# Kernel optimization log

Hardware: AMD Instinct MI355X
Metric: run time of the kernel (lower is better)

Reference implementation:

```python
import jax, jax.numpy as jnp
from jax import lax
import numpy as np

DEPTH = 4
D_MODEL = 192
D_INNER = 384
D_STATE = 16
D_CONV = 4
DT_RANK = 12
STRIDE = 4
NUM_PATCHES = 400
L_SEQ = NUM_PATCHES + 1  # +1 cls token appended at the end
EPS = 1e-5


def _rmsnorm(x, w):
    x = x.astype(jnp.float32)
    return (x * lax.rsqrt(jnp.mean(x * x, axis=-1, keepdims=True) + EPS)) * w


def _mamba(x, in_w, cw, cb, xp_w, dtw, dtb, A_log, Dv, ow):
    # x: [B, L, D_MODEL]
    B = x.shape[0]
    xz = jnp.einsum('bld,ed->ble', x, in_w)            # [B, L, 2*D_INNER]
    u, z = jnp.split(xz, 2, axis=-1)                   # [B, L, D_INNER] each
    # causal depthwise conv over L
    u_t = jnp.transpose(u, (0, 2, 1))                  # [B, D_INNER, L]
    u_pad = jnp.pad(u_t, ((0, 0), (0, 0), (D_CONV - 1, 0)))
    conv = lax.conv_general_dilated(
        u_pad, cw[:, None, :], (1,), 'VALID',
        dimension_numbers=('NCH', 'OIH', 'NCH'),
        feature_group_count=D_INNER)                   # [B, D_INNER, L]
    u = jax.nn.silu(conv + cb[:, None])
    u = jnp.transpose(u, (0, 2, 1))                    # [B, L, D_INNER]
    xdbl = jnp.einsum('bld,ed->ble', u, xp_w)          # [B, L, 44]
    dt, Bm, Cm = jnp.split(xdbl, [DT_RANK, DT_RANK + D_STATE], axis=-1)
    dt = jax.nn.softplus(jnp.einsum('blr,dr->bld', dt, dtw) + dtb)  # [B, L, D_INNER]
    A = -jnp.exp(A_log)                                # [D_INNER, D_STATE]
    dA = jnp.exp(dt[..., None] * A)                    # [B, L, D_INNER, D_STATE]
    dBu = dt[..., None] * Bm[:, :, None, :] * u[..., None]
    h0 = jnp.zeros((B, D_INNER, D_STATE), dtype=dA.dtype)

    def step(h, inp):
        dA_t, dBu_t = inp
        h = dA_t * h + dBu_t
        return h, h

    _, hs = lax.scan(step, h0, (jnp.swapaxes(dA, 0, 1), jnp.swapaxes(dBu, 0, 1)))
    hs = jnp.swapaxes(hs, 0, 1)                        # [B, L, D_INNER, D_STATE]
    y = jnp.einsum('bldn,bln->bld', hs, Cm) + u * Dv
    y = y * jax.nn.silu(z)
    return jnp.einsum('bld,ed->ble', y, ow)            # [B, L, D_MODEL]


def _forward(imgs, patch_w, patch_b, pos_embed, cls_token, norm_w, in_proj_w,
             conv_w, conv_b, xproj_w, dt_w, dt_b, A_log, D_param, out_w,
             normf_w, head_w, head_b):
    B = imgs.shape[0]
    # StrideEmbed: non-overlapping strides of 4 bytes -> linear to embed_dim
    x = imgs.reshape(B, NUM_PATCHES, STRIDE) @ patch_w + patch_b  # [B, 400, 192]
    x = x + pos_embed[:, :-1, :]
    cls = cls_token + pos_embed[:, -1:, :]             # [1, 1, 192]
    x = jnp.concatenate([x, jnp.broadcast_to(cls, (B, 1, D_MODEL))], axis=1)
    hidden = x
    residual = None
    for i in range(DEPTH):
        residual = hidden if residual is None else hidden + residual  # fp32 residual stream
        h = _rmsnorm(residual, norm_w[i])
        hidden = _mamba(h, in_proj_w[i], conv_w[i], conv_b[i], xproj_w[i],
                        dt_w[i], dt_b[i], A_log[i], D_param[i], out_w[i])
    x = _rmsnorm(hidden + residual, normf_w)
    cls_out = x[:, -1, :]                              # [B, 192]
    logits = cls_out @ head_w.T + head_b               # [B, 1000]
    return logits


def setup_inputs() -> dict:
    key = jax.random.key(0)
    ks = jax.random.split(key, 16)
    B = 32
    rn = lambda k, s, sc: jax.random.normal(k, s, dtype=jnp.float32) * sc
    A_log = jnp.broadcast_to(jnp.log(jnp.arange(1.0, D_STATE + 1.0, dtype=jnp.float32)),
                             (DEPTH, D_INNER, D_STATE))
    return {
        'imgs': rn(ks[0], (B, 1, 40, 40), 1.0),
        'patch_w': rn(ks[1], (STRIDE, D_MODEL), 0.1),
        'patch_b': jnp.zeros((D_MODEL,), jnp.float32),
        'pos_embed': rn(ks[2], (1, L_SEQ, D_MODEL), 0.02),
        'cls_token': rn(ks[3], (1, 1, D_MODEL), 0.02),
        'norm_w': jnp.ones((DEPTH, D_MODEL), jnp.float32),
        'in_proj_w': rn(ks[4], (DEPTH, 2 * D_INNER, D_MODEL), 0.05),
        'conv_w': rn(ks[5], (DEPTH, D_INNER, D_CONV), 0.3),
        'conv_b': jnp.zeros((DEPTH, D_INNER), jnp.float32),
        'xproj_w': rn(ks[6], (DEPTH, DT_RANK + 2 * D_STATE, D_INNER), 0.05),
        'dt_w': rn(ks[7], (DEPTH, D_INNER, DT_RANK), 0.1),
        'dt_b': rn(ks[8], (DEPTH, D_INNER), 0.5) - 4.0,
        'A_log': A_log,
        'D_param': jnp.ones((DEPTH, D_INNER), jnp.float32),
        'out_w': rn(ks[9], (DEPTH, D_MODEL, D_INNER), 0.05),
        'normf_w': jnp.ones((D_MODEL,), jnp.float32),
        'head_w': rn(ks[10], (1000, D_MODEL), 0.05),
        'head_b': jnp.zeros((1000,), jnp.float32),
    }


def reference(imgs, patch_w, patch_b, pos_embed, cls_token, norm_w, in_proj_w,
              conv_w, conv_b, xproj_w, dt_w, dt_b, A_log, D_param, out_w,
              normf_w, head_w, head_b):
    return _forward(imgs, patch_w, patch_b, pos_embed, cls_token, norm_w,
                    in_proj_w, conv_w, conv_b, xproj_w, dt_w, dt_b, A_log,
                    D_param, out_w, normf_w, head_w, head_b)
```

## Files before the change

### kernel.cpp

```cpp
#include <hip/hip_runtime.h>
#include <hip/hip_bf16.h>

#define B_SZ 32
#define LSEQ 401
#define NT (B_SZ * LSEQ)
#define DM 192
#define DI 384
#define DS 16
#define EPSF 1e-5f
#define ST 40
#define STP 44
#define NCH 8
#define PQN 1376256

typedef __attribute__((ext_vector_type(8))) short short8;
typedef __attribute__((ext_vector_type(4))) float f32x4;
typedef __hip_bfloat16 bf16;

#define OFF_IMGS    0
#define OFF_PATCHW  51200
#define OFF_PATCHB  51968
#define OFF_POS     52160
#define OFF_CLS     129152
#define OFF_NORMW   129344
#define OFF_INW     130112
#define OFF_CONVW   719936
#define OFF_CONVB   726080
#define OFF_XPROJW  727616
#define OFF_DTW     795200
#define OFF_DTB     813632
#define OFF_ALOG    815168
#define OFF_DP      839744
#define OFF_OUTW    841280
#define OFF_NORMF   1136192
#define OFF_HEADW   1136384
#define OFF_HEADB   1328384
#define OFF_TOTAL   1329384

#define WB_INW   0
#define WB_XPJ   589824
#define WB_OUT   688128
#define WB_DTW   983040
#define WB_TOTAL 1032192

__device__ __forceinline__ int chunk_s(int c) { return c == 0 ? 0 : c * 50 + 1; }
__device__ __forceinline__ int chunk_e(int c) { return (c + 1) * 50 + 1; }

__device__ __forceinline__ float ldsrc(const void* p, int off, int isbf) {
  return isbf ? __bfloat162float(((const bf16*)p)[off]) : ((const float*)p)[off];
}
__device__ __forceinline__ float fast_silu(float z) {
  return z * __builtin_amdgcn_rcpf(1.f + __expf(-z));
}
__device__ __forceinline__ float fast_softplus(float x) {
  float e = __expf(x);
  return (x > 15.f) ? x : __logf(1.f + e);
}

#define DPP_ADD(x, ctrl) \
  x += __int_as_float(__builtin_amdgcn_update_dpp(0, __float_as_int(x), ctrl, 0xF, 0xF, true))
__device__ __forceinline__ float row_sum16(float x) {
  DPP_ADD(x, 0xB1);
  DPP_ADD(x, 0x4E);
  DPP_ADD(x, 0x124);
  DPP_ADD(x, 0x128);
  return x;
}

struct P18 { const void* p[18]; };

__global__ __launch_bounds__(256) void k_convwb(P18 t, float* __restrict__ fin,
                                                bf16* __restrict__ wb) {
  static const int st[19] = {OFF_IMGS, OFF_PATCHW, OFF_PATCHB, OFF_POS, OFF_CLS,
                             OFF_NORMW, OFF_INW, OFF_CONVW, OFF_CONVB, OFF_XPROJW,
                             OFF_DTW, OFF_DTB, OFF_ALOG, OFF_DP, OFF_OUTW,
                             OFF_NORMF, OFF_HEADW, OFF_HEADB, OFF_TOTAL};
  int isbf = (((const unsigned short*)t.p[5])[0] == 0x3F80) ? 1 : 0;
  int idx = blockIdx.x * 256 + threadIdx.x;
  if (idx < OFF_TOTAL) {
    int lo = 0;
#pragma unroll
    for (int i = 1; i < 18; ++i) if (idx >= st[i]) lo = i;
    fin[idx] = ldsrc(t.p[lo], idx - st[lo], isbf);
  } else if (idx < OFF_TOTAL + WB_TOTAL) {
    int j = idx - OFF_TOTAL;
    float v;
    if (j < WB_XPJ) {
      v = ldsrc(t.p[6], j, isbf);
    } else if (j < WB_OUT) {
      int i2 = j - WB_XPJ;
      int l = i2 / (64 * 384);
      int r = (i2 / 384) & 63;
      int k = i2 % 384;
      v = (r < 44) ? ldsrc(t.p[9], l * 44 * 384 + r * 384 + k, isbf) : 0.f;
    } else if (j < WB_DTW) {
      v = ldsrc(t.p[14], j - WB_OUT, isbf);
    } else {
      int i2 = j - WB_DTW;
      int l = i2 / (384 * 32);
      int r = i2 % (384 * 32);
      int d = r >> 5;
      int k = r & 31;
      v = (k < 12) ? ldsrc(t.p[10], l * 4608 + d * 12 + k, isbf) : 0.f;
    }
    wb[j] = __float2bfloat16(v);
  }
}

__device__ __forceinline__ void inproj32(const bf16 (*shb)[200],
                                         const bf16* __restrict__ Win,
                                         bf16* __restrict__ xb,
                                         bf16* __restrict__ zb,
                                         int row0, int tid) {
  int lane = tid & 63, wave = tid >> 6;
  int q = lane >> 4, mlo = lane & 15;
  short8 afrA[6], afrB[6];
#pragma unroll
  for (int kk = 0; kk < 6; ++kk) {
    afrA[kk] = *(const short8*)&shb[mlo][kk * 32 + q * 8];
    afrB[kk] = *(const short8*)&shb[16 + mlo][kk * 32 + q * 8];
  }
  const bf16* wbase = Win + (size_t)(wave * 96 + mlo) * DM + q * 8;
#pragma unroll
  for (int jh = 0; jh < 2; ++jh) {
    short8 Bb[18];
#pragma unroll
    for (int j = 0; j < 3; ++j)
#pragma unroll
      for (int kk = 0; kk < 6; ++kk)
        Bb[j * 6 + kk] = *(const short8*)(wbase + (size_t)(jh * 3 + j) * 16 * DM + kk * 32);
#pragma unroll
    for (int j = 0; j < 3; ++j) {
      f32x4 aA = {}, aB = {};
#pragma unroll
      for (int kk = 0; kk < 6; ++kk) {
        aA = __builtin_amdgcn_mfma_f32_16x16x32_bf16(afrA[kk], Bb[j * 6 + kk], aA, 0, 0, 0);
        aB = __builtin_amdgcn_mfma_f32_16x16x32_bf16(afrB[kk], Bb[j * 6 + kk], aB, 0, 0, 0);
      }
      int n = wave * 96 + (jh * 3 + j) * 16 + mlo;
      if (n < DI) {
#pragma unroll
        for (int i = 0; i < 4; ++i) {
          xb[(size_t)(row0 + q * 4 + i) * DI + n] = __float2bfloat16(aA[i]);
          xb[(size_t)(row0 + 16 + q * 4 + i) * DI + n] = __float2bfloat16(aB[i]);
        }
      } else {
        int nz = n - DI;
#pragma unroll
        for (int i = 0; i < 4; ++i) {
          zb[(size_t)(row0 + q * 4 + i) * DI + nz] = __float2bfloat16(aA[i]);
          zb[(size_t)(row0 + 16 + q * 4 + i) * DI + nz] = __float2bfloat16(aB[i]);
        }
      }
    }
  }
}

__global__ __launch_bounds__(512, 2) void k_embedin(const float* __restrict__ fin,
                                                    float* __restrict__ residual,
                                                    const bf16* __restrict__ Win,
                                                    bf16* __restrict__ xb,
                                                    bf16* __restrict__ zb) {
  __shared__ bf16 shb[32][200];
  const float* imgs = fin + OFF_IMGS;
  const float* pw   = fin + OFF_PATCHW;
  const float* pb   = fin + OFF_PATCHB;
  const float* pos  = fin + OFF_POS;
  const float* cls  = fin + OFF_CLS;
  const float* nw0  = fin + OFF_NORMW;
  int tid = threadIdx.x;
  int row0 = blockIdx.x * 32;
  {
    int row = tid >> 4, g = tid & 15;
    int t = row0 + row;
    int b = t / LSEQ, l = t % LSEQ;
    float im[4];
    if (l < 400) {
#pragma unroll
      for (int s = 0; s < 4; ++s) im[s] = imgs[b * 1600 + l * 4 + s];
    }
    float rn[12], ss = 0.f;
#pragma unroll
    for (int k = 0; k < 12; ++k) {
      int col = g + 16 * k;
      float v;
      if (l < 400) {
        v = pb[col] + pos[l * DM + col];
#pragma unroll
        for (int s = 0; s < 4; ++s) v = fmaf(im[s], pw[s * DM + col], v);
      } else {
        v = cls[col] + pos[400 * DM + col];
      }
      residual[(size_t)t * DM + col] = v;
      rn[k] = v;
      ss = fmaf(v, v, ss);
    }
    ss = row_sum16(ss);
    float sres = rsqrtf(ss / (float)DM + EPSF);
#pragma unroll
    for (int k = 0; k < 12; ++k) {
      int col = g + 16 * k;
      shb[row][col] = __float2bfloat16(rn[k] * sres * nw0[col]);
    }
  }
  __syncthreads();
  inproj32(shb, Win, xb, zb, row0, tid);
}

__global__ __launch_bounds__(512) void k_xdt(const bf16* __restrict__ xb,
                                             const float* __restrict__ cw,
                                             const float* __restrict__ cb,
                                             const bf16* __restrict__ Wbf,
                                             float* __restrict__ xdbl,
                                             const bf16* __restrict__ dtwb,
                                             const float* __restrict__ dtb,
                                             bf16* __restrict__ ub,
                                             bf16* __restrict__ dto) {
  __shared__ bf16  sxt[19][392];
  __shared__ bf16  su[16][392];
  __shared__ float4 scw4[384];
  __shared__ float scb[384];
  __shared__ float sxp[2][16][48];
  __shared__ bf16  sxb[16][32];
  int row0 = blockIdx.x * 16;
  int tid = threadIdx.x;
  for (int i = tid; i < 19 * 48; i += 512) {
    int r = i / 48, c8 = i - r * 48;
    int t = row0 - 3 + r;
    if (t < 0) t = 0;
    *(short8*)&sxt[r][c8 * 8] = *(const short8*)(xb + (size_t)t * DI + c8 * 8);
  }
  for (int i = tid; i < 384; i += 512) {
    scw4[i] = ((const float4*)cw)[i];
    scb[i] = cb[i];
  }
  __syncthreads();
  for (int i = tid; i < 768; i += 512) {
    int tok = i / 48;
    int c8 = i - tok * 48;
    int d0 = c8 * 8;
    int t = row0 + tok;
    int l = t % LSEQ;
    float xr[4][8];
#pragma unroll
    for (int k = 0; k < 4; ++k) {
      short8 v = *(const short8*)&sxt[tok + k][d0];
      bool ok = (l - 3 + k) >= 0;
#pragma unroll
      for (int j = 0; j < 8; ++j) {
        unsigned int uu = ((unsigned int)(unsigned short)v[j]) << 16;
        xr[k][j] = ok ? __uint_as_float(uu) : 0.f;
      }
    }
    short8 uvv;
#pragma unroll
    for (int j = 0; j < 8; ++j) {
      float4 w = scw4[d0 + j];
      float a = scb[d0 + j];
      a = fmaf(xr[0][j], w.x, a);
      a = fmaf(xr[1][j], w.y, a);
      a = fmaf(xr[2][j], w.z, a);
      a = fmaf(xr[3][j], w.w, a);
      bf16 h = __float2bfloat16(fast_silu(a));
      uvv[j] = *reinterpret_cast<short*>(&h);
    }
    *(short8*)&su[tok][d0] = uvv;
    *(short8*)(ub + (size_t)t * DI + d0) = uvv;
  }
  __syncthreads();
  int lane = tid & 63;
  int wave = tid >> 6;
  int q = lane >> 4;
  int mlo = lane & 15;
  if (wave < 6) {
    int colw = (wave % 3) * 16;
    int kh = wave / 3;
    f32x4 acc = {};
    for (int k0 = 0; k0 < 192; k0 += 32) {
      short8 a = *(const short8*)&su[mlo][kh * 192 + k0 + q * 8];
      short8 b = *(const short8*)(Wbf + (size_t)(colw + mlo) * DI + kh * 192 + k0 + q * 8);
      acc = __builtin_amdgcn_mfma_f32_16x16x32_bf16(a, b, acc, 0, 0, 0);
    }
#pragma unroll
    for (int i = 0; i < 4; ++i) sxp[kh][q * 4 + i][colw + mlo] = acc[i];
  }
  __syncthreads();
  for (int i = tid; i < 16 * 44; i += 512) {
    int r = i / 44, c = i - r * 44;
    xdbl[(size_t)(row0 + r) * 44 + c] = sxp[0][r][c] + sxp[1][r][c];
  }
  for (int i = tid; i < 512; i += 512) {
    int tok = i >> 5, k = i & 31;
    sxb[tok][k] = __float2bfloat16(k < 12 ? sxp[0][tok][k] + sxp[1][tok][k] : 0.f);
  }
  __syncthreads();
  short8 afrag = *(const short8*)&sxb[mlo][q * 8];
#pragma unroll
  for (int jt = 0; jt < 3; ++jt) {
    int d = (wave * 3 + jt) * 16 + mlo;
    short8 bfrag = *(const short8*)(dtwb + (size_t)d * 32 + q * 8);
    f32x4 acc = {};
    acc = __builtin_amdgcn_mfma_f32_16x16x32_bf16(afrag, bfrag, acc, 0, 0, 0);
    float dtbv = dtb[d];
#pragma unroll
    for (int i = 0; i < 4; ++i)
      dto[(size_t)(row0 + q * 4 + i) * DI + d] =
          __float2bfloat16(fast_softplus(acc[i] + dtbv));
  }
}

__global__ __launch_bounds__(512) void k_scanA(const bf16* __restrict__ ub,
                                               const bf16* __restrict__ dtv,
                                               const float* __restrict__ xdbl,
                                               const float* __restrict__ A_log,
                                               float* __restrict__ Pq) {
  __shared__ float sdt[32][STP], sw[32][STP], sB[16][STP];
  int bx = blockIdx.x, b = blockIdx.y, c = blockIdx.z;
  int d0 = bx * 32;
  int tid = threadIdx.x;
  int dloc = tid >> 4, n = tid & 15;
  float A = -__expf(A_log[(d0 + dloc) * DS + n]);
  float S = 0.f, h = 0.f;
  int base = b * LSEQ;
  int lt = tid >> 5, lj = tid & 31;
  int s = chunk_s(c), e = chunk_e(c);
  for (int t0 = s; t0 < e; t0 += ST) {
    int tc = min(ST, e - t0);
    for (int tt = lt; tt < tc; tt += 16) {
      int g = base + t0 + tt;
      float dv = __bfloat162float(dtv[(size_t)g * DI + d0 + lj]);
      sdt[lj][tt] = dv;
      sw[lj][tt] = dv * __bfloat162float(ub[(size_t)g * DI + d0 + lj]);
      if (lj < 16) sB[lj][tt] = xdbl[(size_t)g * 44 + 12 + lj];
    }
    __syncthreads();
    int l4 = 0;
    for (; l4 + 4 <= tc; l4 += 4) {
      float4 dt4 = *(const float4*)&sdt[dloc][l4];
      float4 w4  = *(const float4*)&sw[dloc][l4];
      float4 B4  = *(const float4*)&sB[n][l4];
      h = fmaf(__expf(dt4.x * A), h, w4.x * B4.x);
      h = fmaf(__expf(dt4.y * A), h, w4.y * B4.y);
      h = fmaf(__expf(dt4.z * A), h, w4.z * B4.z);
      h = fmaf(__expf(dt4.w * A), h, w4.w * B4.w);
      S += dt4.x + dt4.y + dt4.z + dt4.w;
    }
    for (; l4 < tc; ++l4) {
      float dv = sdt[dloc][l4];
      h = fmaf(__expf(dv * A), h, sw[dloc][l4] * sB[n][l4]);
      S += dv;
    }
    __syncthreads();
  }
  int idx = ((c * B_SZ + b) * 12 + bx) * 512 + tid;
  Pq[idx] = __expf(A * S);
  Pq[PQN + idx] = h;
}

__global__ __launch_bounds__(512) void k_scanB(const bf16* __restrict__ zb,
                                               const bf16* __restrict__ ub,
                                               const bf16* __restrict__ dtv,
                                               const float* __restrict__ xdbl,
                                               const float* __restrict__ A_log,
                                               const float* __restrict__ Dp,
                                               const float* __restrict__ Pq,
                                               bf16* __restrict__ yb) {
  __shared__ float sdt[32][STP], sw[32][STP], sB[16][STP], sC[16][STP],
                   sz[32][STP], sy[32][STP];
  int bx = blockIdx.x, b = blockIdx.y, c = blockIdx.z;
  int d0 = bx * 32;
  int tid = threadIdx.x;
  int dloc = tid >> 4, n = tid & 15;
  float A = -__expf(A_log[(d0 + dloc) * DS + n]);
  float h = 0.f;
  for (int j = 0; j < c; ++j) {
    int idx = ((j * B_SZ + b) * 12 + bx) * 512 + tid;
    h = Pq[PQN + idx] + Pq[idx] * h;
  }
  int base = b * LSEQ;
  int lt = tid >> 5, lj = tid & 31;
  float Dvj = Dp[d0 + lj];
  int s = chunk_s(c), e = chunk_e(c);
  for (int t0 = s; t0 < e; t0 += ST) {
    int tc = min(ST, e - t0);
    for (int tt = lt; tt < tc; tt += 16) {
      int g = base + t0 + tt;
      float dv = __bfloat162float(dtv[(size_t)g * DI + d0 + lj]);
      float uv = __bfloat162float(ub[(size_t)g * DI + d0 + lj]);
      sdt[lj][tt] = dv;
      sw[lj][tt] = dv * uv;
      sy[lj][tt] = uv * Dvj;
      sz[lj][tt] = fast_silu(__bfloat162float(zb[(size_t)g * DI + d0 + lj]));
      if (lj < 32) {
        float v = xdbl[(size_t)g * 44 + 12 + lj];
        if (lj < 16) sB[lj][tt] = v;
        else         sC[lj - 16][tt] = v;
      }
    }
    __syncthreads();
    int l4 = 0;
    for (; l4 + 4 <= tc; l4 += 4) {
      float4 dt4 = *(const float4*)&sdt[dloc][l4];
      float4 w4  = *(const float4*)&sw[dloc][l4];
      float4 B4  = *(const float4*)&sB[n][l4];
      float4 C4  = *(const float4*)&sC[n][l4];
      float c0, c1, c2, c3;
      h = fmaf(__expf(dt4.x * A), h, w4.x * B4.x); c0 = row_sum16(h * C4.x);
      h = fmaf(__expf(dt4.y * A), h, w4.y * B4.y); c1 = row_sum16(h * C4.y);
      h = fmaf(__expf(dt4.z * A), h, w4.z * B4.z); c2 = row_sum16(h * C4.z);
      h = fmaf(__expf(dt4.w * A), h, w4.w * B4.w); c3 = row_sum16(h * C4.w);
      if (n == 0) {
        float4 uD4 = *(const float4*)&sy[dloc][l4];
        float4 z4  = *(const float4*)&sz[dloc][l4];
        float4 yv;
        yv.x = (c0 + uD4.x) * z4.x;
        yv.y = (c1 + uD4.y) * z4.y;
        yv.z = (c2 + uD4.z) * z4.z;
        yv.w = (c3 + uD4.w) * z4.w;
        *(float4*)&sy[dloc][l4] = yv;
      }
    }
    for (; l4 < tc; ++l4) {
      h = fmaf(__expf(sdt[dloc][l4] * A), h, sw[dloc][l4] * sB[n][l4]);
      float cc = row_sum16(h * sC[n][l4]);
      if (n == 0) sy[dloc][l4] = (cc + sy[dloc][l4]) * sz[dloc][l4];
    }
    __syncthreads();
    for (int tt = lt; tt < tc; tt += 16)
      yb[(size_t)(base + t0 + tt) * DI + d0 + lj] = __float2bfloat16(sy[lj][tt]);
    __syncthreads();
  }
}

__global__ __launch_bounds__(512, 2) void k_outin(const bf16* __restrict__ yb,
                                                  const bf16* __restrict__ Wout,
                                                  float* __restrict__ residual,
                                                  const float* __restrict__ nw,
                                                  const bf16* __restrict__ Win,
                                                  bf16* __restrict__ xb,
                                                  bf16* __restrict__ zb) {
  __shared__ float sCt[32][200];
  __shared__ bf16  shb[32][200];
  int tid = threadIdx.x;
  int lane = tid & 63;
  int wave = tid >> 6;
  int row0 = blockIdx.x * 32;
  int q = lane >> 4;
  int mlo = lane & 15;
  {
    int colw = (wave & 3) * 48;
    int rg = (wave >> 2) * 16;
    const bf16* arow = yb + (size_t)(row0 + rg + mlo) * DI + q * 8;
    const bf16* brow = Wout + (size_t)(colw + mlo) * DI + q * 8;
    short8 Af[12], Bf[36];
#pragma unroll
    for (int k = 0; k < 12; ++k) Af[k] = *(const short8*)(arow + k * 32);
#pragma unroll
    for (int j = 0; j < 3; ++j)
#pragma unroll
      for (int k = 0; k < 12; ++k)
        Bf[j * 12 + k] = *(const short8*)(brow + (size_t)j * 16 * DI + k * 32);
    f32x4 acc[3] = {};
#pragma unroll
    for (int k = 0; k < 12; ++k) {
      acc[0] = __builtin_amdgcn_mfma_f32_16x16x32_bf16(Af[k], Bf[k], acc[0], 0, 0, 0);
      acc[1] = __builtin_amdgcn_mfma_f32_16x16x32_bf16(Af[k], Bf[12 + k], acc[1], 0, 0, 0);
      acc[2] = __builtin_amdgcn_mfma_f32_16x16x32_bf16(Af[k], Bf[24 + k], acc[2], 0, 0, 0);
    }
#pragma unroll
    for (int j = 0; j < 3; ++j)
#pragma unroll
      for (int i = 0; i < 4; ++i) sCt[rg + q * 4 + i][colw + j * 16 + mlo] = acc[j][i];
  }
  __syncthreads();
  {
    int row = tid >> 4, g = tid & 15;
    int t = row0 + row;
    float rn[12], ss = 0.f;
#pragma unroll
    for (int k = 0; k < 12; ++k) {
      int col = g + 16 * k;
      float x = sCt[row][col] + residual[(size_t)t * DM + col];
      rn[k] = x;
      ss = fmaf(x, x, ss);
    }
    ss = row_sum16(ss);
    float sres = rsqrtf(ss / (float)DM + EPSF);
#pragma unroll
    for (int k = 0; k < 12; ++k) {
      int col = g + 16 * k;
      residual[(size_t)t * DM + col] = rn[k];
      shb[row][col] = __float2bfloat16(rn[k] * sres * nw[col]);
    }
  }
  __syncthreads();
  inproj32(shb, Win, xb, zb, row0, tid);
}

__global__ __launch_bounds__(256) void k_lastout(const bf16* __restrict__ yb,
                                                 const bf16* __restrict__ Wout,
                                                 const float* __restrict__ resIn,
                                                 float* __restrict__ clsbuf) {
  __shared__ float sCt[16][200];
  int tid = threadIdx.x;
  int lane = tid & 63;
  int wave = tid >> 6;
  int b0 = blockIdx.x * 16;
  int q = lane >> 4;
  int mlo = lane & 15;
  int colw = wave * 48;
  f32x4 acc[3] = {};
  const bf16* arow = yb + ((size_t)(b0 + mlo) * LSEQ + 400) * DI + q * 8;
  for (int k0 = 0; k0 < DI; k0 += 32) {
    short8 a = *(const short8*)(arow + k0);
#pragma unroll
    for (int j = 0; j < 3; ++j) {
      short8 b = *(const short8*)(Wout + (size_t)(colw + j * 16 + mlo) * DI + k0 + q * 8);
      acc[j] = __builtin_amdgcn_mfma_f32_16x16x32_bf16(a, b, acc[j], 0, 0, 0);
    }
  }
#pragma unroll
  for (int j = 0; j < 3; ++j)
#pragma unroll
    for (int i = 0; i < 4; ++i) sCt[q * 4 + i][colw + j * 16 + mlo] = acc[j][i];
  __syncthreads();
  int row = tid >> 4, g = tid & 15;
  int bb = b0 + row;
#pragma unroll
  for (int k = 0; k < 12; ++k) {
    int col = g + 16 * k;
    clsbuf[(size_t)bb * DM + col] =
        sCt[row][col] + resIn[((size_t)bb * LSEQ + 400) * DM + col];
  }
}

__global__ __launch_bounds__(256) void k_final(const float* __restrict__ clsbuf,
                                               const float* __restrict__ fin,
                                               const void* __restrict__ nw_raw,
                                               void* __restrict__ out) {
  const float* normf  = fin + OFF_NORMF;
  const float* head_w = fin + OFF_HEADW;
  const float* head_b = fin + OFF_HEADB;
  __shared__ float clsv[DM];
  __shared__ float partial[4];
  __shared__ float sres;
  int b = blockIdx.x;
  float r = 0.f;
  if (threadIdx.x < DM) r = clsbuf[(size_t)b * DM + threadIdx.x];
  float ss = r * r;
#pragma unroll
  for (int m = 32; m >= 1; m >>= 1) ss += __shfl_xor(ss, m, 64);
  if ((threadIdx.x & 63) == 0) partial[threadIdx.x >> 6] = ss;
  __syncthreads();
  if (threadIdx.x == 0)
    sres = rsqrtf((partial[0] + partial[1] + partial[2] + partial[3]) / (float)DM + EPSF);
  __syncthreads();
  if (threadIdx.x < DM) clsv[threadIdx.x] = r * sres * normf[threadIdx.x];
  __syncthreads();
  int isbf = (((const unsigned short*)nw_raw)[0] == 0x3F80) ? 1 : 0;
  for (int e = threadIdx.x; e < 1000; e += 256) {
    float acc = head_b[e];
    for (int k = 0; k < DM; ++k) acc = fmaf(clsv[k], head_w[e * DM + k], acc);
    if (isbf) ((bf16*)out)[b * 1000 + e] = __float2bfloat16(acc);
    else      ((float*)out)[b * 1000 + e] = acc;
  }
}

extern "C" void kernel_launch(void* const* d_in, const int* in_sizes, int n_in,
                              void* d_out, int out_size, void* d_ws, size_t ws_size,
                              hipStream_t stream) {
  char* base = (char*)d_ws;
  size_t off = 0;
  auto alloc = [&](size_t bytes) { char* p = base + off; off = (off + bytes + 255) & ~(size_t)255; return p; };
  float* fin      = (float*)alloc((size_t)OFF_TOTAL * 4);
  bf16*  wb       = (bf16*)alloc((size_t)WB_TOTAL * 2);
  float* residual = (float*)alloc((size_t)NT * DM * 4);
  bf16*  xb       = (bf16*)alloc((size_t)NT * DI * 2);
  bf16*  zb       = (bf16*)alloc((size_t)NT * DI * 2);
  bf16*  ub       = (bf16*)alloc((size_t)NT * DI * 2);
  float* xdbl     = (float*)alloc((size_t)NT * 44 * 4);
  bf16*  dtb16    = (bf16*)alloc((size_t)NT * DI * 2);
  float* Pq       = (float*)alloc((size_t)2 * PQN * 4);
  float* clsbuf   = (float*)alloc((size_t)B_SZ * DM * 4);
  bf16*  yb       = ub;

  P18 t;
  for (int i = 0; i < 18; ++i) t.p[i] = d_in[i];
  k_convwb<<<(OFF_TOTAL + WB_TOTAL + 255) / 256, 256, 0, stream>>>(t, fin, wb);

  k_embedin<<<NT / 32, 512, 0, stream>>>(fin, residual, wb + WB_INW, xb, zb);

  for (int layer = 0; layer < 4; ++layer) {
    const float* dtb = fin + OFF_DTB + layer * DI;
    const float* alog = fin + OFF_ALOG + layer * DI * DS;

    k_xdt<<<NT / 16, 512, 0, stream>>>(xb, fin + OFF_CONVW + layer * DI * 4,
                                       fin + OFF_CONVB + layer * DI,
                                       wb + WB_XPJ + layer * 64 * DI, xdbl,
                                       wb + WB_DTW + layer * 384 * 32, dtb, ub, dtb16);

    k_scanA<<<dim3(12, B_SZ, NCH - 1), 512, 0, stream>>>(ub, dtb16, xdbl, alog, Pq);
    k_scanB<<<dim3(12, B_SZ, NCH), 512, 0, stream>>>(zb, ub, dtb16, xdbl, alog,
                                                     fin + OFF_DP + layer * DI, Pq, yb);

    if (layer < 3) {
      k_outin<<<NT / 32, 512, 0, stream>>>(yb, wb + WB_OUT + layer * DM * DI, residual,
                                           fin + OFF_NORMW + (layer + 1) * DM,
                                           wb + WB_INW + (layer + 1) * 768 * DM, xb, zb);
    } else {
      k_lastout<<<2, 256, 0, stream>>>(yb, wb + WB_OUT + 3 * DM * DI, residual, clsbuf);
    }
  }
  k_final<<<B_SZ, 256, 0, stream>>>(clsbuf, fin, d_in[5], d_out);
}
```

Baseline: 593.2 us.

## Stage out-proj A tile in LDS, split K across waves, vectorize residual access

In k_outin, the 32x384 y tile is loaded cooperatively into shared memory once. Each wave now computes both 16-row groups over half of K, instead of each wave loading its own A rows directly from global memory with the full K. The two K-half partial sums are reduced through a doubled sCt buffer. Residual reads and writes switch to float4 with a contiguous 12-column-per-thread mapping, and launch bounds use amdgpu_waves_per_eu(2,2) in place of min-blocks. This cuts per-wave B-fragment registers and redundant global A loads, but raises LDS usage and may add LDS bank conflicts.

After: 568.9 us. 4.1% less time.

```diff
diff --git a/kernel.cpp b/kernel.cpp
--- a/kernel.cpp
+++ b/kernel.cpp
@@ -156,11 +156,13 @@
   }
 }
 
-__global__ __launch_bounds__(512, 2) void k_embedin(const float* __restrict__ fin,
-                                                    float* __restrict__ residual,
-                                                    const bf16* __restrict__ Win,
-                                                    bf16* __restrict__ xb,
-                                                    bf16* __restrict__ zb) {
+__global__ __launch_bounds__(512)
+__attribute__((amdgpu_waves_per_eu(2, 2)))
+void k_embedin(const float* __restrict__ fin,
+               float* __restrict__ residual,
+               const bf16* __restrict__ Win,
+               bf16* __restrict__ xb,
+               bf16* __restrict__ zb) {
   __shared__ bf16 shb[32][200];
   const float* imgs = fin + OFF_IMGS;
   const float* pw   = fin + OFF_PATCHW;
@@ -432,14 +434,17 @@
   }
 }
 
-__global__ __launch_bounds__(512, 2) void k_outin(const bf16* __restrict__ yb,
-                                                  const bf16* __restrict__ Wout,
-                                                  float* __restrict__ residual,
-                                                  const float* __restrict__ nw,
-                                                  const bf16* __restrict__ Win,
-                                                  bf16* __restrict__ xb,
-                                                  bf16* __restrict__ zb) {
-  __shared__ float sCt[32][200];
+__global__ __launch_bounds__(512)
+__attribute__((amdgpu_waves_per_eu(2, 2)))
+void k_outin(const bf16* __restrict__ yb,
+             const bf16* __restrict__ Wout,
+             float* __restrict__ residual,
+             const float* __restrict__ nw,
+             const bf16* __restrict__ Win,
+             bf16* __restrict__ xb,
+             bf16* __restrict__ zb) {
+  __shared__ bf16  syt[32][392];
+  __shared__ float sCt[2][32][200];
   __shared__ bf16  shb[32][200];
   int tid = threadIdx.x;
   int lane = tid & 63;
@@ -448,48 +453,77 @@
   int q = lane >> 4;
   int mlo = lane & 15;
   {
+    int i0 = tid, i1 = tid + 512, i2 = tid + 1024;
+    const bf16* src = yb + (size_t)row0 * DI;
+    short8 v0 = *(const short8*)(src + (i0 / 48) * DI + (i0 % 48) * 8);
+    short8 v1 = *(const short8*)(src + (i1 / 48) * DI + (i1 % 48) * 8);
+    short8 v2 = *(const short8*)(src + (i2 / 48) * DI + (i2 % 48) * 8);
+    *(short8*)&syt[i0 / 48][(i0 % 48) * 8] = v0;
+    *(short8*)&syt[i1 / 48][(i1 % 48) * 8] = v1;
+    *(short8*)&syt[i2 / 48][(i2 % 48) * 8] = v2;
+  }
+  __syncthreads();
+  {
     int colw = (wave & 3) * 48;
-    int rg = (wave >> 2) * 16;
-    const bf16* arow = yb + (size_t)(row0 + rg + mlo) * DI + q * 8;
-    const bf16* brow = Wout + (size_t)(colw + mlo) * DI + q * 8;
-    short8 Af[12], Bf[36];
-#pragma unroll
-    for (int k = 0; k < 12; ++k) Af[k] = *(const short8*)(arow + k * 32);
+    int kh = wave >> 2;
+    const bf16* brow = Wout + (size_t)(colw + mlo) * DI + kh * 192 + q * 8;
+    short8 Bf[18];
 #pragma unroll
     for (int j = 0; j < 3; ++j)
 #pragma unroll
-      for (int k = 0; k < 12; ++k)
-        Bf[j * 12 + k] = *(const short8*)(brow + (size_t)j * 16 * DI + k * 32);
-    f32x4 acc[3] = {};
-#pragma unroll
-    for (int k = 0; k < 12; ++k) {
-      acc[0] = __builtin_amdgcn_mfma_f32_16x16x32_bf16(Af[k], Bf[k], acc[0], 0, 0, 0);
-      acc[1] = __builtin_amdgcn_mfma_f32_16x16x32_bf16(Af[k], Bf[12 + k], acc[1], 0, 0, 0);
-      acc[2] = __builtin_amdgcn_mfma_f32_16x16x32_bf16(Af[k], Bf[24 + k], acc[2], 0, 0, 0);
-    }
-#pragma unroll
-    for (int j = 0; j < 3; ++j)
-#pragma unroll
-      for (int i = 0; i < 4; ++i) sCt[rg + q * 4 + i][colw + j * 16 + mlo] = acc[j][i];
+      for (int k2 = 0; k2 < 6; ++k2)
+        Bf[j * 6 + k2] = *(const short8*)(brow + (size_t)j * 16 * DI + k2 * 32);
+    short8 afA[6], afB[6];
+#pragma unroll
+    for (int k2 = 0; k2 < 6; ++k2) {
+      afA[k2] = *(const short8*)&syt[mlo][kh * 192 + k2 * 32 + q * 8];
+      afB[k2] = *(const short8*)&syt[16 + mlo][kh * 192 + k2 * 32 + q * 8];
+    }
+    f32x4 acc[2][3] = {};
+#pragma unroll
+    for (int k2 = 0; k2 < 6; ++k2) {
+#pragma unroll
+      for (int j = 0; j < 3; ++j) {
+        acc[0][j] = __builtin_amdgcn_mfma_f32_16x16x32_bf16(afA[k2], Bf[j * 6 + k2], acc[0][j], 0, 0, 0);
+        acc[1][j] = __builtin_amdgcn_mfma_f32_16x16x32_bf16(afB[k2], Bf[j * 6 + k2], acc[1][j], 0, 0, 0);
+      }
+    }
+#pragma unroll
+    for (int rg = 0; rg < 2; ++rg)
+#pragma unroll
+      for (int j = 0; j < 3; ++j)
+#pragma unroll
+        for (int i = 0; i < 4; ++i)
+          sCt[kh][rg * 16 + q * 4 + i][colw + j * 16 + mlo] = acc[rg][j][i];
   }
   __syncthreads();
   {
     int row = tid >> 4, g = tid & 15;
     int t = row0 + row;
+    float* rp = residual + (size_t)t * DM + g * 12;
+    float4 r4[3];
+#pragma unroll
+    for (int j = 0; j < 3; ++j) r4[j] = *(const float4*)(rp + j * 4);
     float rn[12], ss = 0.f;
 #pragma unroll
     for (int k = 0; k < 12; ++k) {
-      int col = g + 16 * k;
-      float x = sCt[row][col] + residual[(size_t)t * DM + col];
+      int col = g * 12 + k;
+      float x = sCt[0][row][col] + sCt[1][row][col] + ((const float*)r4)[k];
       rn[k] = x;
       ss = fmaf(x, x, ss);
     }
     ss = row_sum16(ss);
     float sres = rsqrtf(ss / (float)DM + EPSF);
 #pragma unroll
+    for (int j = 0; j < 3; ++j) {
+      float4 w4;
+      w4.x = rn[j * 4 + 0]; w4.y = rn[j * 4 + 1];
+      w4.z = rn[j * 4 + 2]; w4.w = rn[j * 4 + 3];
+      *(float4*)(rp + j * 4) = w4;
+    }
+#pragma unroll
     for (int k = 0; k < 12; ++k) {
-      int col = g + 16 * k;
-      residual[(size_t)t * DM + col] = rn[k];
+      int col = g * 12 + k;
       shb[row][col] = __float2bfloat16(rn[k] * sres * nw[col]);
     }
   }
```
